# Kernel tuning notes

Measured on AMD Instinct MI355X. Metric: run time of the kernel, lower is better.

The kernel has to match this reference:

```python
import jax, jax.numpy as jnp
import numpy as np

B, C, H, W = 8, 256, 192, 192
INTERNAL = 16


def setup_inputs() -> dict:
    key = jax.random.key(0)
    k1, k2, k3, k4, k5 = jax.random.split(key, 5)
    inputs = jax.random.normal(k1, (B, C, H, W), dtype=jnp.float32)
    w_down = jax.random.normal(k2, (INTERNAL, C), dtype=jnp.float32) * 0.05
    b_down = jax.random.normal(k3, (INTERNAL,), dtype=jnp.float32) * 0.05
    w_up = jax.random.normal(k4, (C, INTERNAL), dtype=jnp.float32) * 0.05
    b_up = jax.random.normal(k5, (C,), dtype=jnp.float32) * 0.05
    return {"inputs": inputs, "w_down": w_down, "b_down": b_down,
            "w_up": w_up, "b_up": b_up}


def reference(inputs, w_down, b_down, w_up, b_up):
    # Squeeze: L2 norm over spatial dims -> [B, C]
    Gx = jnp.sqrt(jnp.sum(inputs * inputs, axis=(2, 3)))  # [B, C]
    # torch: Gx.mean(dim=-1, keepdim=True) acts on the trailing size-1 dim
    # of the [B, C, 1, 1] tensor, so it is just Gx itself.
    x = Gx / (Gx + 1e-6)  # [B, C]
    # 1x1 convs on a [B, C, 1, 1] tensor == dense matmuls on [B, C]
    h = jax.nn.relu(x @ w_down.T + b_down)          # [B, INTERNAL]
    gate = jax.nn.sigmoid(h @ w_up.T + b_up)        # [B, C]
    return inputs * gate[:, :, None, None]
```

## Files before the change

### kernel.cpp

```cpp
#include <hip/hip_runtime.h>
#include <math.h>

#define BB 8
#define CC 256
#define HWSZ 36864
#define HW4 9216
#define TPB 256
#define IT 36
#define INTERNAL 16
#define NSLICE (BB * CC)

typedef float f4 __attribute__((ext_vector_type(4)));

__global__ __launch_bounds__(TPB) void se_sumsq_kernel(
    const float* __restrict__ in, float* __restrict__ sumsq)
{
    const int bc = blockIdx.x;
    const f4* p = reinterpret_cast<const f4*>(in + (size_t)bc * HWSZ);

    float a0 = 0.f, a1 = 0.f, a2 = 0.f, a3 = 0.f;
    #pragma unroll
    for (int i = 0; i < IT; i += 4) {
        f4 v0 = p[threadIdx.x + (i + 0) * TPB];
        f4 v1 = p[threadIdx.x + (i + 1) * TPB];
        f4 v2 = p[threadIdx.x + (i + 2) * TPB];
        f4 v3 = p[threadIdx.x + (i + 3) * TPB];
        a0 += v0.x * v0.x + v0.y * v0.y + v0.z * v0.z + v0.w * v0.w;
        a1 += v1.x * v1.x + v1.y * v1.y + v1.z * v1.z + v1.w * v1.w;
        a2 += v2.x * v2.x + v2.y * v2.y + v2.z * v2.z + v2.w * v2.w;
        a3 += v3.x * v3.x + v3.y * v3.y + v3.z * v3.z + v3.w * v3.w;
    }
    float acc = (a0 + a1) + (a2 + a3);
    for (int off = 32; off > 0; off >>= 1)
        acc += __shfl_down(acc, off, 64);

    __shared__ float red[4];
    const int lane = threadIdx.x & 63, wave = threadIdx.x >> 6;
    if (lane == 0) red[wave] = acc;
    __syncthreads();
    if (threadIdx.x == 0)
        sumsq[bc] = red[0] + red[1] + red[2] + red[3];
}

__global__ __launch_bounds__(TPB) void se_scale_kernel(
    const float* __restrict__ in,
    const float* __restrict__ sumsq,
    const float* __restrict__ w_down,
    const float* __restrict__ b_down,
    const float* __restrict__ w_up,
    const float* __restrict__ b_up,
    float* __restrict__ out)
{
    const int s = (NSLICE - 1) - blockIdx.x;
    const int b = s >> 8;
    const int c = s & 255;
    const int tid = threadIdx.x;

    __shared__ float xs[CC];
    __shared__ float hs[INTERNAL];
    __shared__ float gsh;

    {
        float g = sqrtf(sumsq[(b << 8) + tid]);
        xs[tid] = g / (g + 1e-6f);
    }
    __syncthreads();

    {
        const int j = tid >> 4, l = tid & 15;
        const float* wr = w_down + j * CC;
        float a = 0.f;
        #pragma unroll
        for (int k = 0; k < CC / 16; ++k)
            a += xs[l + k * 16] * wr[l + k * 16];
        a += __shfl_down(a, 8, 16);
        a += __shfl_down(a, 4, 16);
        a += __shfl_down(a, 2, 16);
        a += __shfl_down(a, 1, 16);
        if (l == 0) hs[j] = fmaxf(a + b_down[j], 0.f);
    }
    __syncthreads();

    if (tid == 0) {
        float a = b_up[c];
        const float* wu = w_up + c * INTERNAL;
        #pragma unroll
        for (int j = 0; j < INTERNAL; ++j) a += hs[j] * wu[j];
        gsh = 1.f / (1.f + expf(-a));
    }
    __syncthreads();

    const float gv = gsh;
    const f4* pi = reinterpret_cast<const f4*>(in + (size_t)s * HWSZ);
    f4* po = reinterpret_cast<f4*>(out + (size_t)s * HWSZ);

    #pragma unroll
    for (int i = 0; i < IT; i += 4) {
        f4 v0 = __builtin_nontemporal_load(pi + tid + (i + 0) * TPB);
        f4 v1 = __builtin_nontemporal_load(pi + tid + (i + 1) * TPB);
        f4 v2 = __builtin_nontemporal_load(pi + tid + (i + 2) * TPB);
        f4 v3 = __builtin_nontemporal_load(pi + tid + (i + 3) * TPB);
        v0 *= gv; v1 *= gv; v2 *= gv; v3 *= gv;
        __builtin_nontemporal_store(v0, po + tid + (i + 0) * TPB);
        __builtin_nontemporal_store(v1, po + tid + (i + 1) * TPB);
        __builtin_nontemporal_store(v2, po + tid + (i + 2) * TPB);
        __builtin_nontemporal_store(v3, po + tid + (i + 3) * TPB);
    }
}

extern "C" void kernel_launch(void* const* d_in, const int* in_sizes, int n_in,
                              void* d_out, int out_size, void* d_ws, size_t ws_size,
                              hipStream_t stream) {
    const float* inputs = (const float*)d_in[0];
    const float* w_down = (const float*)d_in[1];
    const float* b_down = (const float*)d_in[2];
    const float* w_up   = (const float*)d_in[3];
    const float* b_up   = (const float*)d_in[4];
    float* out   = (float*)d_out;
    float* sumsq = (float*)d_ws;

    se_sumsq_kernel<<<NSLICE, TPB, 0, stream>>>(inputs, sumsq);
    se_scale_kernel<<<NSLICE, TPB, 0, stream>>>(inputs, sumsq,
                                                w_down, b_down, w_up, b_up,
                                                out);
}
```

Measured before the change: 144.1 us.

## Fuse reduction and scaling into one cooperative kernel with per-batch counters

```diff
diff --git a/kernel.cpp b/kernel.cpp
--- a/kernel.cpp
+++ b/kernel.cpp
@@ -4,64 +4,74 @@
 #define BB 8
 #define CC 256
 #define HWSZ 36864
-#define HW4 9216
 #define TPB 256
 #define IT 36
 #define INTERNAL 16
-#define NSLICE (BB * CC)
+#define NSLICE 2048
+#define NBLK 1024
 
 typedef float f4 __attribute__((ext_vector_type(4)));
 
-__global__ __launch_bounds__(TPB) void se_sumsq_kernel(
-    const float* __restrict__ in, float* __restrict__ sumsq)
-{
-    const int bc = blockIdx.x;
-    const f4* p = reinterpret_cast<const f4*>(in + (size_t)bc * HWSZ);
-
+__device__ __forceinline__ float slice_sumsq(const float* __restrict__ in,
+                                             int s, int tid)
+{
+    const f4* p = reinterpret_cast<const f4*>(in + (size_t)s * HWSZ);
     float a0 = 0.f, a1 = 0.f, a2 = 0.f, a3 = 0.f;
     #pragma unroll
     for (int i = 0; i < IT; i += 4) {
-        f4 v0 = p[threadIdx.x + (i + 0) * TPB];
-        f4 v1 = p[threadIdx.x + (i + 1) * TPB];
-        f4 v2 = p[threadIdx.x + (i + 2) * TPB];
-        f4 v3 = p[threadIdx.x + (i + 3) * TPB];
+        f4 v0 = p[tid + (i + 0) * TPB];
+        f4 v1 = p[tid + (i + 1) * TPB];
+        f4 v2 = p[tid + (i + 2) * TPB];
+        f4 v3 = p[tid + (i + 3) * TPB];
         a0 += v0.x * v0.x + v0.y * v0.y + v0.z * v0.z + v0.w * v0.w;
         a1 += v1.x * v1.x + v1.y * v1.y + v1.z * v1.z + v1.w * v1.w;
         a2 += v2.x * v2.x + v2.y * v2.y + v2.z * v2.z + v2.w * v2.w;
         a3 += v3.x * v3.x + v3.y * v3.y + v3.z * v3.z + v3.w * v3.w;
     }
-    float acc = (a0 + a1) + (a2 + a3);
+    return (a0 + a1) + (a2 + a3);
+}
+
+__device__ __forceinline__ void produce(const float* __restrict__ in,
+                                        float* __restrict__ sumsq,
+                                        unsigned int* __restrict__ cnt,
+                                        int s, int tid, int lane, int wave,
+                                        float* red)
+{
+    float acc = slice_sumsq(in, s, tid);
     for (int off = 32; off > 0; off >>= 1)
         acc += __shfl_down(acc, off, 64);
-
-    __shared__ float red[4];
-    const int lane = threadIdx.x & 63, wave = threadIdx.x >> 6;
     if (lane == 0) red[wave] = acc;
     __syncthreads();
-    if (threadIdx.x == 0)
-        sumsq[bc] = red[0] + red[1] + red[2] + red[3];
-}
-
-__global__ __launch_bounds__(TPB) void se_scale_kernel(
-    const float* __restrict__ in,
-    const float* __restrict__ sumsq,
-    const float* __restrict__ w_down,
-    const float* __restrict__ b_down,
-    const float* __restrict__ w_up,
-    const float* __restrict__ b_up,
-    float* __restrict__ out)
-{
-    const int s = (NSLICE - 1) - blockIdx.x;
-    const int b = s >> 8;
-    const int c = s & 255;
-    const int tid = threadIdx.x;
-
-    __shared__ float xs[CC];
-    __shared__ float hs[INTERNAL];
-    __shared__ float gsh;
-
-    {
-        float g = sqrtf(sumsq[(b << 8) + tid]);
+    if (tid == 0) {
+        float tot = red[0] + red[1] + red[2] + red[3];
+        __hip_atomic_store(&sumsq[s], tot, __ATOMIC_RELAXED,
+                           __HIP_MEMORY_SCOPE_AGENT);
+        __hip_atomic_fetch_add(&cnt[s >> 8], 1u, __ATOMIC_RELEASE,
+                               __HIP_MEMORY_SCOPE_AGENT);
+    }
+    __syncthreads();
+}
+
+__device__ __forceinline__ float gate_for(const float* __restrict__ sumsq,
+                                          const unsigned int* __restrict__ cnt,
+                                          const float* __restrict__ w_down,
+                                          const float* __restrict__ b_down,
+                                          const float* __restrict__ w_up,
+                                          const float* __restrict__ b_up,
+                                          int b, int c, int tid,
+                                          float* xs, float* hs, float* gsh)
+{
+    if (tid == 0) {
+        while (__hip_atomic_load(&cnt[b], __ATOMIC_ACQUIRE,
+                                 __HIP_MEMORY_SCOPE_AGENT) < (unsigned)CC)
+            __builtin_amdgcn_s_sleep(8);
+    }
+    __syncthreads();
+
+    {
+        float ss = __hip_atomic_load(&sumsq[(b << 8) + tid], __ATOMIC_RELAXED,
+                                     __HIP_MEMORY_SCOPE_AGENT);
+        float g = sqrtf(ss);
         xs[tid] = g / (g + 1e-6f);
     }
     __syncthreads();
@@ -86,14 +96,18 @@
         const float* wu = w_up + c * INTERNAL;
         #pragma unroll
         for (int j = 0; j < INTERNAL; ++j) a += hs[j] * wu[j];
-        gsh = 1.f / (1.f + expf(-a));
-    }
-    __syncthreads();
-
-    const float gv = gsh;
+        *gsh = 1.f / (1.f + expf(-a));
+    }
+    __syncthreads();
+    return *gsh;
+}
+
+__device__ __forceinline__ void scale_store(const float* __restrict__ in,
+                                            float* __restrict__ out,
+                                            float gv, int s, int tid)
+{
     const f4* pi = reinterpret_cast<const f4*>(in + (size_t)s * HWSZ);
     f4* po = reinterpret_cast<f4*>(out + (size_t)s * HWSZ);
-
     #pragma unroll
     for (int i = 0; i < IT; i += 4) {
         f4 v0 = __builtin_nontemporal_load(pi + tid + (i + 0) * TPB);
@@ -108,6 +122,98 @@
     }
 }
 
+__global__ __launch_bounds__(TPB, 4) void se_onepass_kernel(
+    const float* __restrict__ in, float* __restrict__ out,
+    float* __restrict__ sumsq,
+    unsigned int* __restrict__ cnt,
+    const float* __restrict__ w_down, const float* __restrict__ b_down,
+    const float* __restrict__ w_up, const float* __restrict__ b_up)
+{
+    const int blk = blockIdx.x;
+    const int tid = threadIdx.x;
+    const int lane = tid & 63, wave = tid >> 6;
+
+    __shared__ float red[4];
+    __shared__ float xs[CC];
+    __shared__ float hs[INTERNAL];
+    __shared__ float gsh;
+
+    const int sA = blk;
+    const int sB = blk + NBLK;
+
+    produce(in, sumsq, cnt, sA, tid, lane, wave, red);
+    produce(in, sumsq, cnt, sB, tid, lane, wave, red);
+
+    float gA = gate_for(sumsq, cnt, w_down, b_down, w_up, b_up,
+                        sA >> 8, sA & 255, tid, xs, hs, &gsh);
+    scale_store(in, out, gA, sA, tid);
+
+    float gB = gate_for(sumsq, cnt, w_down, b_down, w_up, b_up,
+                        sB >> 8, sB & 255, tid, xs, hs, &gsh);
+    scale_store(in, out, gB, sB, tid);
+}
+
+__global__ __launch_bounds__(TPB) void se_sumsq_kernel(
+    const float* __restrict__ in, float* __restrict__ sumsq)
+{
+    const int bc = blockIdx.x;
+    float acc = slice_sumsq(in, bc, threadIdx.x);
+    for (int off = 32; off > 0; off >>= 1)
+        acc += __shfl_down(acc, off, 64);
+    __shared__ float red[4];
+    const int lane = threadIdx.x & 63, wave = threadIdx.x >> 6;
+    if (lane == 0) red[wave] = acc;
+    __syncthreads();
+    if (threadIdx.x == 0)
+        sumsq[bc] = red[0] + red[1] + red[2] + red[3];
+}
+
+__global__ __launch_bounds__(TPB) void se_scale_kernel(
+    const float* __restrict__ in,
+    const float* __restrict__ sumsq,
+    const float* __restrict__ w_down, const float* __restrict__ b_down,
+    const float* __restrict__ w_up, const float* __restrict__ b_up,
+    float* __restrict__ out)
+{
+    const int s = (NSLICE - 1) - blockIdx.x;
+    const int b = s >> 8;
+    const int c = s & 255;
+    const int tid = threadIdx.x;
+
+    __shared__ float xs[CC];
+    __shared__ float hs[INTERNAL];
+    __shared__ float gsh;
+
+    {
+        float g = sqrtf(sumsq[(b << 8) + tid]);
+        xs[tid] = g / (g + 1e-6f);
+    }
+    __syncthreads();
+    {
+        const int j = tid >> 4, l = tid & 15;
+        const float* wr = w_down + j * CC;
+        float a = 0.f;
+        #pragma unroll
+        for (int k = 0; k < CC / 16; ++k)
+            a += xs[l + k * 16] * wr[l + k * 16];
+        a += __shfl_down(a, 8, 16);
+        a += __shfl_down(a, 4, 16);
+        a += __shfl_down(a, 2, 16);
+        a += __shfl_down(a, 1, 16);
+        if (l == 0) hs[j] = fmaxf(a + b_down[j], 0.f);
+    }
+    __syncthreads();
+    if (tid == 0) {
+        float a = b_up[c];
+        const float* wu = w_up + c * INTERNAL;
+        #pragma unroll
+        for (int j = 0; j < INTERNAL; ++j) a += hs[j] * wu[j];
+        gsh = 1.f / (1.f + expf(-a));
+    }
+    __syncthreads();
+    scale_store(in, out, gsh, s, tid);
+}
+
 extern "C" void kernel_launch(void* const* d_in, const int* in_sizes, int n_in,
                               void* d_out, int out_size, void* d_ws, size_t ws_size,
                               hipStream_t stream) {
@@ -116,11 +222,23 @@
     const float* b_down = (const float*)d_in[2];
     const float* w_up   = (const float*)d_in[3];
     const float* b_up   = (const float*)d_in[4];
-    float* out   = (float*)d_out;
-    float* sumsq = (float*)d_ws;
-
-    se_sumsq_kernel<<<NSLICE, TPB, 0, stream>>>(inputs, sumsq);
-    se_scale_kernel<<<NSLICE, TPB, 0, stream>>>(inputs, sumsq,
-                                                w_down, b_down, w_up, b_up,
-                                                out);
-}
+    float* out = (float*)d_out;
+
+    float* sumsq      = (float*)d_ws;
+    unsigned int* cnt = (unsigned int*)(sumsq + NSLICE);
+
+    hipMemsetAsync(cnt, 0, BB * sizeof(unsigned int), stream);
+
+    void* args[] = { (void*)&inputs, (void*)&out, (void*)&sumsq, (void*)&cnt,
+                     (void*)&w_down, (void*)&b_down, (void*)&w_up, (void*)&b_up };
+    hipError_t err = hipLaunchCooperativeKernel(
+        reinterpret_cast<void*>(se_onepass_kernel),
+        dim3(NBLK), dim3(TPB), args, 0, stream);
+
+    if (err != hipSuccess) {
+        se_sumsq_kernel<<<NSLICE, TPB, 0, stream>>>(inputs, sumsq);
+        se_scale_kernel<<<NSLICE, TPB, 0, stream>>>(inputs, sumsq,
+                                                    w_down, b_down, w_up, b_up,
+                                                    out);
+    }
+}
```

After: 284.0 us. +97.1%, slower.
